# Kernel tuning notes

Hardware: AMD Instinct MI355X
Metric: run time of the kernel (lower is better)

Reference implementation:

```python
import jax, jax.numpy as jnp
import numpy as np
from jax import lax

DIM = 128
EXP = 4
K = 7
B, D, H, W = 2, 48, 48, 48


def setup_inputs() -> dict:
    key = jax.random.key(0)
    ks = jax.random.split(key, 8)
    C, Ch = DIM, EXP * DIM
    x = jax.random.normal(ks[0], (B, C, D, H, W), dtype=jnp.float32)
    dw_w = jax.random.normal(ks[1], (C, 1, K, K, K), dtype=jnp.float32) * 0.05
    dw_b = jnp.zeros((C,), dtype=jnp.float32)
    ln_g = jnp.ones((C,), dtype=jnp.float32)
    ln_b = jnp.zeros((C,), dtype=jnp.float32)
    w1 = jax.random.normal(ks[2], (C, Ch), dtype=jnp.float32) * (1.0 / np.sqrt(C))
    b1 = jnp.zeros((Ch,), dtype=jnp.float32)
    grn_g = jnp.zeros((Ch,), dtype=jnp.float32)
    grn_b = jnp.zeros((Ch,), dtype=jnp.float32)
    w2 = jax.random.normal(ks[3], (Ch, C), dtype=jnp.float32) * (1.0 / np.sqrt(Ch))
    b2 = jnp.zeros((C,), dtype=jnp.float32)
    return {"x": x, "dw_w": dw_w, "dw_b": dw_b, "ln_g": ln_g, "ln_b": ln_b,
            "w1": w1, "b1": b1, "grn_g": grn_g, "grn_b": grn_b, "w2": w2, "b2": b2}


def reference(x, dw_w, dw_b, ln_g, ln_b, w1, b1, grn_g, grn_b, w2, b2):
    C = x.shape[1]
    pad = (K - 1) // 2
    # depthwise 3D conv, NCDHW
    y = lax.conv_general_dilated(
        x, dw_w, window_strides=(1, 1, 1),
        padding=[(pad, pad)] * 3,
        feature_group_count=C,
        dimension_numbers=("NCDHW", "OIDHW", "NCDHW"))
    y = y + dw_b[None, :, None, None, None]
    y = jnp.transpose(y, (0, 2, 3, 4, 1))  # [B,D,H,W,C] channels-last
    # LayerNorm over channels (eps=1e-6)
    mu = jnp.mean(y, axis=-1, keepdims=True)
    var = jnp.mean((y - mu) ** 2, axis=-1, keepdims=True)
    y = (y - mu) / jnp.sqrt(var + 1e-6) * ln_g + ln_b
    # pwconv1 + GELU (exact)
    h = jax.nn.gelu(jnp.einsum("bdhwc,ce->bdhwe", y, w1) + b1, approximate=False)
    # GRN: global L2 over spatial dims per channel, divisive norm over channel mean
    gx = jnp.sqrt(jnp.sum(h * h, axis=(1, 2, 3), keepdims=True))  # [B,1,1,1,Ch]
    nx = gx / (jnp.mean(gx, axis=-1, keepdims=True) + 1e-6)
    h = grn_g * (h * nx) + grn_b + h
    # pwconv2
    y = jnp.einsum("bdhwe,ec->bdhwc", h, w2) + b2
    y = jnp.transpose(y, (0, 4, 1, 2, 3))  # back to NCDHW
    return x + y
```

## Files before the change

kernel.cpp:

```cpp
#include <hip/hip_runtime.h>
#include <math.h>

#define PVOX 110592
#define CDIM 128
#define EDIM 512

typedef __attribute__((ext_vector_type(8))) short short8_t;
typedef __attribute__((ext_vector_type(4))) float float4_t;

__device__ __forceinline__ unsigned short f2bf(float f) {
  unsigned int u = __float_as_uint(f);
  unsigned int r = (u + 0x7FFFu + ((u >> 16) & 1u)) >> 16;
  return (unsigned short)r;
}
__device__ __forceinline__ float bf2f(unsigned short s) {
  return __uint_as_float(((unsigned int)s) << 16);
}
__device__ __forceinline__ int swz(int row, int col) {
  return (row << 7) + ((((col >> 3) ^ (row & 15)) << 3) | (col & 7));
}
__device__ __forceinline__ int swzO(int c, int p) {
  return (c << 7) + (p ^ ((c & 15) << 2));
}

__global__ __launch_bounds__(256) void k0_wprep(
    const float* __restrict__ w1, const float* __restrict__ w2,
    unsigned short* __restrict__ w1t, unsigned short* __restrict__ w2t) {
  int idx = blockIdx.x * 256 + threadIdx.x;
  int e = idx >> 7, c = idx & 127;
  w1t[e * 128 + c] = f2bf(w1[c * 512 + e]);
  w2t[c * 512 + e] = f2bf(w2[e * 128 + c]);
}

__global__ __launch_bounds__(384) void k1_dwconv(
    const float* __restrict__ x, const float* __restrict__ dw_w,
    const float* __restrict__ dw_b, float* __restrict__ yconv) {
  __shared__ float sx[22 * 14 * 60];
  int bx = blockIdx.x;
  int ht = bx % 6;  int tmp = bx / 6;
  int dtile = tmp % 3; tmp /= 3;
  int c = tmp & 127; int b = tmp >> 7;
  int d0 = dtile * 16, h0 = ht * 8;
  const float* xp = x + (size_t)(b * 128 + c) * PVOX;
  int t = threadIdx.x;
  for (int i = t; i < 4312; i += 384) {
    int gi = i % 14; int rr = i / 14; int hh = rr % 14; int r = rr / 14;
    int gd = d0 - 3 + r, gh = h0 - 3 + hh;
    float4_t v = {0.f, 0.f, 0.f, 0.f};
    if ((unsigned)gd < 48u && (unsigned)gh < 48u && gi >= 1 && gi <= 12)
      v = *(const float4_t*)&xp[(gd * 48 + gh) * 48 + gi * 4 - 4];
    *(float4_t*)&sx[r * 840 + hh * 60 + gi * 4] = v;
  }
  __syncthreads();
  int wc = t % 6; int h = (t / 6) % 8; int dt = t / 48;
  int w0 = wc * 8;
  const float* wbase = dw_w + c * 343;
  float bias = dw_b[c];
  float a0[8], a1[8];
#pragma unroll
  for (int i = 0; i < 8; i++) { a0[i] = bias; a1[i] = bias; }
  for (int kh = 0; kh < 7; kh++) {
    int hl = h + kh;
    const float* hp = &sx[hl * 60 + w0];
#pragma unroll
    for (int r8 = 0; r8 < 8; r8++) {
      int r = 2 * dt + r8;
      const float* rp = &hp[r * 840];
      float4_t v4[4];
#pragma unroll
      for (int g = 0; g < 4; g++) v4[g] = *(const float4_t*)&rp[g * 4];
      if (r8 <= 6) {
        const float* wr = wbase + r8 * 49 + kh * 7;
#pragma unroll
        for (int kw = 0; kw < 7; kw++) {
          float wv = wr[kw];
#pragma unroll
          for (int wi = 0; wi < 8; wi++) {
            int vi = wi + kw + 1;
            a0[wi] += wv * v4[vi >> 2][vi & 3];
          }
        }
      }
      if (r8 >= 1) {
        const float* wr = wbase + (r8 - 1) * 49 + kh * 7;
#pragma unroll
        for (int kw = 0; kw < 7; kw++) {
          float wv = wr[kw];
#pragma unroll
          for (int wi = 0; wi < 8; wi++) {
            int vi = wi + kw + 1;
            a1[wi] += wv * v4[vi >> 2][vi & 3];
          }
        }
      }
    }
  }
  int dg = d0 + 2 * dt;
  float* op0 = yconv + (size_t)(b * 128 + c) * PVOX + ((size_t)dg * 48 + (h0 + h)) * 48 + w0;
  float* op1 = op0 + 48 * 48;
  float4_t o;
  o[0] = a0[0]; o[1] = a0[1]; o[2] = a0[2]; o[3] = a0[3]; *(float4_t*)&op0[0] = o;
  o[0] = a0[4]; o[1] = a0[5]; o[2] = a0[6]; o[3] = a0[7]; *(float4_t*)&op0[4] = o;
  o[0] = a1[0]; o[1] = a1[1]; o[2] = a1[2]; o[3] = a1[3]; *(float4_t*)&op1[0] = o;
  o[0] = a1[4]; o[1] = a1[5]; o[2] = a1[6]; o[3] = a1[7]; *(float4_t*)&op1[4] = o;
}

__global__ __launch_bounds__(256) void k2_ln(
    const float* __restrict__ yconv, const float* __restrict__ ln_g,
    const float* __restrict__ ln_b, unsigned short* __restrict__ ycl) {
  __shared__ float sy[128 * 65];
  __shared__ float smean[64], srstd[64];
  int bx = blockIdx.x;
  int b = bx / 1728;
  int p0 = (bx % 1728) * 64;
  int t = threadIdx.x;
  int v = t & 63, c4 = t >> 6;
  const float* yp = yconv + (size_t)b * 128 * PVOX + p0;
  for (int cc = 0; cc < 32; cc++) {
    int c = cc * 4 + c4;
    sy[c * 65 + v] = yp[(size_t)c * PVOX + v];
  }
  __syncthreads();
  if (t < 64) {
    float s = 0.f, ss = 0.f;
    for (int c = 0; c < 128; c++) { float val = sy[c * 65 + t]; s += val; ss += val * val; }
    float mu = s * (1.f / 128.f);
    float var = ss * (1.f / 128.f) - mu * mu;
    smean[t] = mu; srstd[t] = rsqrtf(var + 1e-6f);
  }
  __syncthreads();
  unsigned short* op = ycl + ((size_t)b * PVOX + p0) * 128;
  for (int it = 0; it < 32; it++) {
    int idx = it * 256 + t;
    int vv = idx >> 7, c = idx & 127;
    float val = (sy[c * 65 + vv] - smean[vv]) * srstd[vv] * ln_g[c] + ln_b[c];
    op[vv * 128 + c] = f2bf(val);
  }
}

__global__ __launch_bounds__(256) void k3_pw1(
    const unsigned short* __restrict__ ycl, const unsigned short* __restrict__ w1t,
    const float* __restrict__ b1, unsigned short* __restrict__ h,
    float* __restrict__ gsum) {
  __shared__ short smem[2 * 128 * 128];
  short* sA = smem;
  short* sB = smem + 128 * 128;
  int bx = blockIdx.x;
  int et = bx & 3; int pt = bx >> 2;
  int e0 = et << 7;
  int b = (pt >= 864) ? 1 : 0;
  int t = threadIdx.x;
  for (int it = 0; it < 8; it++) {
    int flat = it * 2048 + t * 8;
    int row = flat >> 7, col = flat & 127;
    *(uint4*)&sA[swz(row, col)] = *(const uint4*)&ycl[((size_t)(pt * 128 + row)) * 128 + col];
    *(uint4*)&sB[swz(row, col)] = *(const uint4*)&w1t[(e0 + row) * 128 + col];
  }
  __syncthreads();
  int wave = t >> 6, lane = t & 63;
  int wm = (wave >> 1) * 64, wn = (wave & 1) * 64;
  int ln15 = lane & 15, q = lane >> 4;
  float4_t acc[4][4] = {};
  for (int kk = 0; kk < 4; kk++) {
    int k0 = kk * 32 + q * 8;
    short8_t af[4], bf[4];
#pragma unroll
    for (int i = 0; i < 4; i++)
      af[i] = *(const short8_t*)&sA[swz(wm + i * 16 + ln15, k0)];
#pragma unroll
    for (int j = 0; j < 4; j++)
      bf[j] = *(const short8_t*)&sB[swz(wn + j * 16 + ln15, k0)];
#pragma unroll
    for (int i = 0; i < 4; i++)
#pragma unroll
      for (int j = 0; j < 4; j++)
        acc[i][j] = __builtin_amdgcn_mfma_f32_16x16x32_bf16(af[i], bf[j], acc[i][j], 0, 0, 0);
  }
  __syncthreads();
  float biasv[4];
#pragma unroll
  for (int j = 0; j < 4; j++) biasv[j] = b1[e0 + wn + j * 16 + ln15];
  float ssq[4] = {0.f, 0.f, 0.f, 0.f};
#pragma unroll
  for (int i = 0; i < 4; i++) {
#pragma unroll
    for (int j = 0; j < 4; j++) {
      int e_local = wn + j * 16 + ln15;
#pragma unroll
      for (int r = 0; r < 4; r++) {
        float val = acc[i][j][r] + biasv[j];
        float g = 0.5f * val * (1.0f + erff(val * 0.70710678118f));
        ssq[j] += g * g;
        sA[swz(wm + i * 16 + q * 4 + r, e_local)] = (short)f2bf(g);
      }
    }
  }
#pragma unroll
  for (int j = 0; j < 4; j++) {
    ssq[j] += __shfl_xor(ssq[j], 16);
    ssq[j] += __shfl_xor(ssq[j], 32);
  }
  if (q == 0) {
#pragma unroll
    for (int j = 0; j < 4; j++)
      atomicAdd(&gsum[b * 512 + e0 + wn + j * 16 + ln15], ssq[j]);
  }
  __syncthreads();
  for (int it = 0; it < 8; it++) {
    int flat = it * 2048 + t * 8;
    int row = flat >> 7, col = flat & 127;
    *(uint4*)&h[((size_t)(pt * 128 + row)) * 512 + e0 + col] = *(const uint4*)&sA[swz(row, col)];
  }
}

__global__ __launch_bounds__(512) void k4_grn(
    const float* __restrict__ gsum, const float* __restrict__ grn_g,
    const float* __restrict__ grn_b, const float* __restrict__ w2,
    const float* __restrict__ b2, float* __restrict__ s, float* __restrict__ badd) {
  __shared__ float red[512];
  int t = threadIdx.x;
  for (int b = 0; b < 2; b++) {
    float gx = sqrtf(gsum[b * 512 + t]);
    red[t] = gx;
    __syncthreads();
    for (int off = 256; off > 0; off >>= 1) {
      if (t < off) red[t] += red[t + off];
      __syncthreads();
    }
    float mean = red[0] * (1.f / 512.f);
    __syncthreads();
    s[b * 512 + t] = 1.0f + grn_g[t] * (gx / (mean + 1e-6f));
  }
  if (t < 128) {
    float acc = b2[t];
    for (int e = 0; e < 512; e++) acc += grn_b[e] * w2[e * 128 + t];
    badd[t] = acc;
  }
}

__global__ __launch_bounds__(256) void k5_pw2(
    const unsigned short* __restrict__ h, const unsigned short* __restrict__ w2t,
    const float* __restrict__ s, const float* __restrict__ badd,
    const float* __restrict__ x, float* __restrict__ out) {
  __shared__ short smem[2 * 128 * 128];
  short* sA = smem;
  short* sB = smem + 128 * 128;
  int bx = blockIdx.x;
  int b = bx / 864;
  int p0 = (bx % 864) * 128;
  int vp0 = bx * 128;
  int t = threadIdx.x;
  int wave = t >> 6, lane = t & 63;
  int wm = (wave >> 1) * 64, wn = (wave & 1) * 64;
  int ln15 = lane & 15, q = lane >> 4;
  const float* sb = s + b * 512;
  float4_t acc[4][4] = {};
  for (int ec = 0; ec < 4; ec++) {
    int e0 = ec * 128;
    for (int it = 0; it < 8; it++) {
      int flat = it * 2048 + t * 8;
      int row = flat >> 7, col = flat & 127;
      uint4 raw = *(const uint4*)&h[((size_t)(vp0 + row)) * 512 + e0 + col];
      const unsigned short* us = (const unsigned short*)&raw;
      unsigned short ov[8];
#pragma unroll
      for (int i2 = 0; i2 < 8; i2++)
        ov[i2] = f2bf(bf2f(us[i2]) * sb[e0 + col + i2]);
      *(uint4*)&sA[swz(row, col)] = *(const uint4*)ov;
      *(uint4*)&sB[swz(row, col)] = *(const uint4*)&w2t[row * 512 + e0 + col];
    }
    __syncthreads();
    for (int kk = 0; kk < 4; kk++) {
      int k0 = kk * 32 + q * 8;
      short8_t af[4], bf[4];
#pragma unroll
      for (int i = 0; i < 4; i++)
        af[i] = *(const short8_t*)&sA[swz(wm + i * 16 + ln15, k0)];
#pragma unroll
      for (int j = 0; j < 4; j++)
        bf[j] = *(const short8_t*)&sB[swz(wn + j * 16 + ln15, k0)];
#pragma unroll
      for (int i = 0; i < 4; i++)
#pragma unroll
        for (int j = 0; j < 4; j++)
          acc[i][j] = __builtin_amdgcn_mfma_f32_16x16x32_bf16(af[i], bf[j], acc[i][j], 0, 0, 0);
    }
    __syncthreads();
  }
  float* sO = (float*)smem;
#pragma unroll
  for (int i = 0; i < 4; i++)
#pragma unroll
    for (int j = 0; j < 4; j++) {
      int c = wn + j * 16 + ln15;
#pragma unroll
      for (int r = 0; r < 4; r++)
        sO[swzO(c, wm + i * 16 + q * 4 + r)] = acc[i][j][r];
    }
  __syncthreads();
  for (int it = 0; it < 16; it++) {
    int flat4 = it * 256 + t;
    int c = flat4 >> 5, col4 = (flat4 & 31) * 4;
    float4_t v = *(const float4_t*)&sO[swzO(c, col4)];
    float bd = badd[c];
    size_t gi = (size_t)(b * 128 + c) * PVOX + p0 + col4;
    float4_t xv = *(const float4_t*)&x[gi];
    v[0] += bd + xv[0]; v[1] += bd + xv[1]; v[2] += bd + xv[2]; v[3] += bd + xv[3];
    *(float4_t*)&out[gi] = v;
  }
}

extern "C" void kernel_launch(void* const* d_in, const int* in_sizes, int n_in,
                              void* d_out, int out_size, void* d_ws, size_t ws_size,
                              hipStream_t stream) {
  (void)in_sizes; (void)n_in; (void)out_size; (void)ws_size;
  const float* x    = (const float*)d_in[0];
  const float* dw_w = (const float*)d_in[1];
  const float* dw_b = (const float*)d_in[2];
  const float* ln_g = (const float*)d_in[3];
  const float* ln_b = (const float*)d_in[4];
  const float* w1   = (const float*)d_in[5];
  const float* b1   = (const float*)d_in[6];
  const float* grn_g= (const float*)d_in[7];
  const float* grn_b= (const float*)d_in[8];
  const float* w2   = (const float*)d_in[9];
  const float* b2   = (const float*)d_in[10];
  float* outp = (float*)d_out;

  char* w = (char*)d_ws;
  float*          yconv = (float*)(w);
  unsigned short* ycl   = (unsigned short*)(w + 113246208);
  unsigned short* h     = (unsigned short*)(w + 169869312);
  float*          gsum  = (float*)(w + 396361728);
  float*          s     = (float*)(w + 396365824);
  float*          badd  = (float*)(w + 396369920);
  unsigned short* w1t   = (unsigned short*)(w + 396370432);
  unsigned short* w2t   = (unsigned short*)(w + 396501504);

  hipMemsetAsync(gsum, 0, 2 * 512 * sizeof(float), stream);
  k0_wprep<<<256, 256, 0, stream>>>(w1, w2, w1t, w2t);
  k1_dwconv<<<4608, 384, 0, stream>>>(x, dw_w, dw_b, yconv);
  k2_ln<<<3456, 256, 0, stream>>>(yconv, ln_g, ln_b, ycl);
  k3_pw1<<<6912, 256, 0, stream>>>(ycl, w1t, b1, h, gsum);
  k4_grn<<<1, 512, 0, stream>>>(gsum, grn_g, grn_b, w2, b2, s, badd);
  k5_pw2<<<1728, 256, 0, stream>>>(h, w2t, s, badd, x, outp);
}
```

Before: 1.021 ms.

## Stream depthwise conv along depth with rolling accumulators and double-buffered planes

The depthwise 7x7x7 conv kernel now has each block own one channel and half of the depth range, instead of loading a 3D halo tile per small output tile. It streams one input depth plane at a time into a double-buffered LDS slab and prefetches the next plane into registers while computing. Each loaded plane feeds seven rolling accumulator rows, one per kd tap, which shift every step, so each input plane is read once instead of once per overlapping depth halo. The cost is a much smaller grid (512 blocks of 384 threads), a barrier per plane, and high register pressure from 42 accumulators, which may reduce latency hiding.

```diff
diff --git a/kernel.cpp b/kernel.cpp
--- a/kernel.cpp
+++ b/kernel.cpp
@@ -35,74 +35,118 @@
 __global__ __launch_bounds__(384) void k1_dwconv(
     const float* __restrict__ x, const float* __restrict__ dw_w,
     const float* __restrict__ dw_b, float* __restrict__ yconv) {
-  __shared__ float sx[22 * 14 * 60];
+  __shared__ float buf[2][3240];
   int bx = blockIdx.x;
-  int ht = bx % 6;  int tmp = bx / 6;
-  int dtile = tmp % 3; tmp /= 3;
-  int c = tmp & 127; int b = tmp >> 7;
-  int d0 = dtile * 16, h0 = ht * 8;
+  int d0 = (bx & 1) * 24;
+  int c = (bx >> 1) & 127;
+  int b = bx >> 8;
   const float* xp = x + (size_t)(b * 128 + c) * PVOX;
-  int t = threadIdx.x;
-  for (int i = t; i < 4312; i += 384) {
-    int gi = i % 14; int rr = i / 14; int hh = rr % 14; int r = rr / 14;
-    int gd = d0 - 3 + r, gh = h0 - 3 + hh;
-    float4_t v = {0.f, 0.f, 0.f, 0.f};
-    if ((unsigned)gd < 48u && (unsigned)gh < 48u && gi >= 1 && gi <= 12)
-      v = *(const float4_t*)&xp[(gd * 48 + gh) * 48 + gi * 4 - 4];
-    *(float4_t*)&sx[r * 840 + hh * 60 + gi * 4] = v;
-  }
-  __syncthreads();
-  int wc = t % 6; int h = (t / 6) % 8; int dt = t / 48;
-  int w0 = wc * 8;
   const float* wbase = dw_w + c * 343;
   float bias = dw_b[c];
-  float a0[8], a1[8];
-#pragma unroll
-  for (int i = 0; i < 8; i++) { a0[i] = bias; a1[i] = bias; }
-  for (int kh = 0; kh < 7; kh++) {
-    int hl = h + kh;
-    const float* hp = &sx[hl * 60 + w0];
-#pragma unroll
-    for (int r8 = 0; r8 < 8; r8++) {
-      int r = 2 * dt + r8;
-      const float* rp = &hp[r * 840];
-      float4_t v4[4];
-#pragma unroll
-      for (int g = 0; g < 4; g++) v4[g] = *(const float4_t*)&rp[g * 4];
-      if (r8 <= 6) {
-        const float* wr = wbase + r8 * 49 + kh * 7;
+  int t = threadIdx.x;
+  int wc = t & 7, h = t >> 3;
+  int w0 = wc * 6;
+  float a[7][6];
+#pragma unroll
+  for (int j = 0; j < 7; j++)
+#pragma unroll
+    for (int wi = 0; wi < 6; wi++) a[j][wi] = bias;
+
+  int zs = d0 - 3; if (zs < 0) zs = 0;
+  int ze = d0 + 26; if (ze > 47) ze = 47;
+
+  {
+    const float* xz = xp + zs * 2304;
+#pragma unroll
+    for (int k = 0; k < 3; k++) {
+      int i = t + 384 * k;
+      if (i < 810) {
+        int r = i / 15, gi = i % 15;
+        int gh = r - 3, gw = gi * 4 - 4;
+        float4_t v = {0.f, 0.f, 0.f, 0.f};
+        if ((unsigned)gh < 48u && gi >= 1 && gi <= 12)
+          v = *(const float4_t*)&xz[gh * 48 + gw];
+        *(float4_t*)&buf[zs & 1][r * 60 + gi * 4] = v;
+      }
+    }
+  }
+  __syncthreads();
+
+  for (int z = zs; z <= ze; z++) {
+    int p = z & 1;
+    float4_t pre[3];
+    bool more = (z < ze);
+    if (more) {
+      const float* xz = xp + (z + 1) * 2304;
+#pragma unroll
+      for (int k = 0; k < 3; k++) {
+        int i = t + 384 * k;
+        pre[k] = (float4_t){0.f, 0.f, 0.f, 0.f};
+        if (i < 810) {
+          int r = i / 15, gi = i % 15;
+          int gh = r - 3, gw = gi * 4 - 4;
+          if ((unsigned)gh < 48u && gi >= 1 && gi <= 12)
+            pre[k] = *(const float4_t*)&xz[gh * 48 + gw];
+        }
+      }
+    }
+    const float* pb = buf[p];
+#pragma unroll
+    for (int kh = 0; kh < 7; kh++) {
+      const float* rp = &pb[(h + kh) * 60 + w0];
+      float v[14];
+#pragma unroll
+      for (int j = 0; j < 14; j++) v[j] = rp[j];
+#pragma unroll
+      for (int kd = 0; kd < 7; kd++) {
+        const float* wr = wbase + kd * 49 + kh * 7;
 #pragma unroll
         for (int kw = 0; kw < 7; kw++) {
           float wv = wr[kw];
 #pragma unroll
-          for (int wi = 0; wi < 8; wi++) {
-            int vi = wi + kw + 1;
-            a0[wi] += wv * v4[vi >> 2][vi & 3];
-          }
+          for (int wi = 0; wi < 6; wi++)
+            a[kd][wi] = fmaf(wv, v[wi + kw + 1], a[kd][wi]);
         }
       }
-      if (r8 >= 1) {
-        const float* wr = wbase + (r8 - 1) * 49 + kh * 7;
-#pragma unroll
-        for (int kw = 0; kw < 7; kw++) {
-          float wv = wr[kw];
-#pragma unroll
-          for (int wi = 0; wi < 8; wi++) {
-            int vi = wi + kw + 1;
-            a1[wi] += wv * v4[vi >> 2][vi & 3];
-          }
+    }
+    if (more) {
+      float* db = buf[p ^ 1];
+#pragma unroll
+      for (int k = 0; k < 3; k++) {
+        int i = t + 384 * k;
+        if (i < 810) {
+          int r = i / 15, gi = i % 15;
+          *(float4_t*)&db[r * 60 + gi * 4] = pre[k];
         }
       }
     }
-  }
-  int dg = d0 + 2 * dt;
-  float* op0 = yconv + (size_t)(b * 128 + c) * PVOX + ((size_t)dg * 48 + (h0 + h)) * 48 + w0;
-  float* op1 = op0 + 48 * 48;
-  float4_t o;
-  o[0] = a0[0]; o[1] = a0[1]; o[2] = a0[2]; o[3] = a0[3]; *(float4_t*)&op0[0] = o;
-  o[0] = a0[4]; o[1] = a0[5]; o[2] = a0[6]; o[3] = a0[7]; *(float4_t*)&op0[4] = o;
-  o[0] = a1[0]; o[1] = a1[1]; o[2] = a1[2]; o[3] = a1[3]; *(float4_t*)&op1[0] = o;
-  o[0] = a1[4]; o[1] = a1[5]; o[2] = a1[6]; o[3] = a1[7]; *(float4_t*)&op1[4] = o;
+    int d = z - 3;
+    if (d >= d0) {
+      float* op = yconv + (size_t)(b * 128 + c) * PVOX + (d * 48 + h) * 48 + w0;
+      float2 o;
+      o.x = a[6][0]; o.y = a[6][1]; *(float2*)&op[0] = o;
+      o.x = a[6][2]; o.y = a[6][3]; *(float2*)&op[2] = o;
+      o.x = a[6][4]; o.y = a[6][5]; *(float2*)&op[4] = o;
+    }
+#pragma unroll
+    for (int j = 6; j >= 1; j--)
+#pragma unroll
+      for (int wi = 0; wi < 6; wi++) a[j][wi] = a[j - 1][wi];
+#pragma unroll
+    for (int wi = 0; wi < 6; wi++) a[0][wi] = bias;
+    __syncthreads();
+  }
+  if (d0 == 24) {
+#pragma unroll
+    for (int m = 0; m < 3; m++) {
+      int d = 45 + m;
+      float* op = yconv + (size_t)(b * 128 + c) * PVOX + (d * 48 + h) * 48 + w0;
+      float2 o;
+      o.x = a[6 - m][0]; o.y = a[6 - m][1]; *(float2*)&op[0] = o;
+      o.x = a[6 - m][2]; o.y = a[6 - m][3]; *(float2*)&op[2] = o;
+      o.x = a[6 - m][4]; o.y = a[6 - m][5]; *(float2*)&op[4] = o;
+    }
+  }
 }
 
 __global__ __launch_bounds__(256) void k2_ln(
@@ -339,7 +383,7 @@
 
   hipMemsetAsync(gsum, 0, 2 * 512 * sizeof(float), stream);
   k0_wprep<<<256, 256, 0, stream>>>(w1, w2, w1t, w2t);
-  k1_dwconv<<<4608, 384, 0, stream>>>(x, dw_w, dw_b, yconv);
+  k1_dwconv<<<512, 384, 0, stream>>>(x, dw_w, dw_b, yconv);
   k2_ln<<<3456, 256, 0, stream>>>(yconv, ln_g, ln_b, ycl);
   k3_pw1<<<6912, 256, 0, stream>>>(ycl, w1t, b1, h, gsum);
   k4_grn<<<1, 512, 0, stream>>>(gsum, grn_g, grn_b, w2, b2, s, badd);
```

Measured after the change: 1.310 ms. +28.3%, slower.
